# Optimization experiments

Measured on AMD Instinct MI355X. Metric: run time of the kernel, lower is better.

The kernel has to match this reference:

```python
import jax, jax.numpy as jnp
import numpy as np

B, T, D = 8, 2048, 1024
DK, DV = 1024, 1024


def setup_inputs() -> dict:
    key = jax.random.key(0)
    ks = jax.random.split(key, 7)
    s = 1.0 / np.sqrt(D)
    return {
        "X": jax.random.normal(ks[0], (B, T, D), dtype=jnp.float32),
        "Wq": jax.random.uniform(ks[1], (D, DK), jnp.float32, -s, s),
        "bq": jax.random.uniform(ks[2], (DK,), jnp.float32, -s, s),
        "Wk": jax.random.uniform(ks[3], (D, DK), jnp.float32, -s, s),
        "bk": jax.random.uniform(ks[4], (DK,), jnp.float32, -s, s),
        "Wv": jax.random.uniform(ks[5], (D, DV), jnp.float32, -s, s),
        "bv": jax.random.uniform(ks[6], (DV,), jnp.float32, -s, s),
    }


def reference(X, Wq, bq, Wk, bk, Wv, bv):
    # relu-activated projections (note: original applies relu to Q, K, V; no 1/sqrt(d) scaling)
    Q = jax.nn.relu(jnp.einsum("btd,dk->btk", X, Wq) + bq)  # [B,T,DK]
    K = jax.nn.relu(jnp.einsum("btd,dk->btk", X, Wk) + bk)  # [B,T,DK]
    V = jax.nn.relu(jnp.einsum("btd,dv->btv", X, Wv) + bv)  # [B,T,DV]
    scores = jnp.einsum("btk,bsk->bts", Q, K)               # [B,T,S] query t attends over keys s
    attn = jax.nn.softmax(scores, axis=-1)
    return jnp.einsum("bts,bsv->btv", attn, V)              # [B,T,DV]
```

## Files before the change

kernel.cpp:

```cpp
#include <hip/hip_runtime.h>

typedef __bf16 bf16x8 __attribute__((ext_vector_type(8)));
typedef _Float16 f16x8 __attribute__((ext_vector_type(8)));
typedef float floatx4 __attribute__((ext_vector_type(4)));

__device__ __forceinline__ unsigned short f2bf(float f) {
  unsigned int u = __float_as_uint(f);
  u += 0x7FFFu + ((u >> 16) & 1u);
  return (unsigned short)(u >> 16);
}
__device__ __forceinline__ unsigned short f2h(float f) {
  _Float16 h = (_Float16)f;
  return __builtin_bit_cast(unsigned short, h);
}
template <bool F16>
__device__ __forceinline__ unsigned short f2x(float f) {
  return F16 ? f2h(f) : f2bf(f);
}

__device__ __forceinline__ void g2l16(const void* g, void* l) {
  __builtin_amdgcn_global_load_lds(
      (const __attribute__((address_space(1))) void*)g,
      (__attribute__((address_space(3))) void*)l, 16, 0, 0);
}

template <int MODE, bool AF32, bool INF16, bool OUTF16>
__global__ __launch_bounds__(256) void gemm_bt(
    const void* __restrict__ Av, int lda, long sA,
    const unsigned short* __restrict__ B, int ldb, long sB,
    void* __restrict__ Cv, int ldc, long sC,
    int K, const float* __restrict__ bias, float* __restrict__ lrow) {
  __shared__ unsigned short As[2][128 * 64];
  __shared__ unsigned short Bs[2][128 * 64];
  const int tid = threadIdx.x;
  const int wave = tid >> 6, lane = tid & 63;
  const int z = blockIdx.z;
  const unsigned short* A16 = (const unsigned short*)Av + (size_t)z * sA;
  const float* A32 = (const float*)Av + (size_t)z * sA;
  B += (size_t)z * sB;

  int bx = blockIdx.x, by = blockIdx.y;
  {
    const int nwg = gridDim.x * gridDim.y;
    if ((nwg & 7) == 0) {
      int flat = by * gridDim.x + bx;
      flat = (flat & 7) * (nwg >> 3) + (flat >> 3);
      bx = flat % gridDim.x;
      by = flat / gridDim.x;
    }
  }
  const int m0 = by * 128, n0 = bx * 128;
  const int wr = (wave >> 1) * 64;
  const int wc = (wave & 1) * 64;
  const int qr = lane >> 4, lr = lane & 15;
  floatx4 acc[4][4] = {};

  auto stageAB = [&](int t, int buf) {
    const int k0 = t << 6;
#pragma unroll
    for (int it = 0; it < 4; ++it) {
      const int base = it * 256 + wave * 64;
      const int idx = base + lane;
      const int row = idx >> 3;
      const int gs = (idx & 7) ^ (row & 7);
      g2l16(A16 + (size_t)(m0 + row) * lda + k0 + gs * 8, &As[buf][base * 8]);
    }
#pragma unroll
    for (int it = 0; it < 4; ++it) {
      const int base = it * 256 + wave * 64;
      const int idx = base + lane;
      const int row = idx >> 3;
      const int gs = (idx & 7) ^ (row & 7);
      g2l16(B + (size_t)(n0 + row) * ldb + k0 + gs * 8, &Bs[buf][base * 8]);
    }
  };

  auto computeT = [&](int buf) {
#pragma unroll
    for (int kk = 0; kk < 64; kk += 32) {
      const int slot = (kk >> 3) + qr;
      if (INF16) {
        f16x8 af[4], bf[4];
#pragma unroll
        for (int i = 0; i < 4; ++i) {
          const int ra = wr + i * 16 + lr;
          af[i] = *(const f16x8*)&As[buf][ra * 64 + ((slot ^ (ra & 7)) * 8)];
        }
#pragma unroll
        for (int j = 0; j < 4; ++j) {
          const int rb = wc + j * 16 + lr;
          bf[j] = *(const f16x8*)&Bs[buf][rb * 64 + ((slot ^ (rb & 7)) * 8)];
        }
#pragma unroll
        for (int i = 0; i < 4; ++i)
#pragma unroll
          for (int j = 0; j < 4; ++j)
            acc[i][j] = __builtin_amdgcn_mfma_f32_16x16x32_f16(
                bf[j], af[i], acc[i][j], 0, 0, 0);
      } else {
        bf16x8 af[4], bf[4];
#pragma unroll
        for (int i = 0; i < 4; ++i) {
          const int ra = wr + i * 16 + lr;
          af[i] = *(const bf16x8*)&As[buf][ra * 64 + ((slot ^ (ra & 7)) * 8)];
        }
#pragma unroll
        for (int j = 0; j < 4; ++j) {
          const int rb = wc + j * 16 + lr;
          bf[j] = *(const bf16x8*)&Bs[buf][rb * 64 + ((slot ^ (rb & 7)) * 8)];
        }
#pragma unroll
        for (int i = 0; i < 4; ++i)
#pragma unroll
          for (int j = 0; j < 4; ++j)
            acc[i][j] = __builtin_amdgcn_mfma_f32_16x16x32_bf16(
                bf[j], af[i], acc[i][j], 0, 0, 0);
      }
    }
  };

  if (!AF32) {
    const int nk = K >> 6;
    stageAB(0, 0);
    for (int t = 0; t < nk; ++t) {
      const int cur = t & 1;
      if (t + 1 < nk) {
        stageAB(t + 1, cur ^ 1);
        asm volatile("s_waitcnt vmcnt(8)" ::: "memory");
      } else {
        asm volatile("s_waitcnt vmcnt(0)" ::: "memory");
      }
      __builtin_amdgcn_sched_barrier(0);
      __builtin_amdgcn_s_barrier();
      __builtin_amdgcn_sched_barrier(0);
      computeT(cur);
      __builtin_amdgcn_sched_barrier(0);
      __builtin_amdgcn_s_barrier();
      __builtin_amdgcn_sched_barrier(0);
    }
  } else {
    for (int k0 = 0; k0 < K; k0 += 64) {
      __syncthreads();
#pragma unroll
      for (int it = 0; it < 8; ++it) {
        const int idx = it * 256 + tid;
        const int row = idx >> 4, c4 = idx & 15;
        float4 v =
            *(const float4*)(A32 + (size_t)(m0 + row) * lda + k0 + c4 * 4);
        const int soff = (((c4 >> 1) ^ (row & 7)) * 2 + (c4 & 1)) * 4;
        *(ushort4*)&As[0][row * 64 + soff] =
            make_ushort4(f2x<INF16>(v.x), f2x<INF16>(v.y), f2x<INF16>(v.z),
                         f2x<INF16>(v.w));
      }
#pragma unroll
      for (int it = 0; it < 4; ++it) {
        const int base = it * 256 + wave * 64;
        const int idx = base + lane;
        const int row = idx >> 3;
        const int gs = (idx & 7) ^ (row & 7);
        g2l16(B + (size_t)(n0 + row) * ldb + k0 + gs * 8, &Bs[0][base * 8]);
      }
      __syncthreads();
      computeT(0);
    }
  }

  float* Cf = (float*)Cv + (size_t)z * sC;
  unsigned short* Cb = (unsigned short*)Cv + (size_t)z * sC;
#pragma unroll
  for (int i = 0; i < 4; ++i) {
    const int row = m0 + wr + i * 16 + lr;
    float rowsum = 0.0f;
    float invl = 1.0f;
    if (MODE == 2) invl = 1.0f / lrow[(size_t)z * 2048 + row];
#pragma unroll
    for (int j = 0; j < 4; ++j) {
      const int col0 = n0 + wc + j * 16 + qr * 4;
      if (MODE == 0) {
        float4 bj = *(const float4*)(bias + col0);
        float v0 = fmaxf(acc[i][j][0] + bj.x, 0.0f);
        float v1 = fmaxf(acc[i][j][1] + bj.y, 0.0f);
        float v2 = fmaxf(acc[i][j][2] + bj.z, 0.0f);
        float v3 = fmaxf(acc[i][j][3] + bj.w, 0.0f);
        *(ushort4*)&Cb[(size_t)row * ldc + col0] =
            make_ushort4(f2x<OUTF16>(v0), f2x<OUTF16>(v1), f2x<OUTF16>(v2),
                         f2x<OUTF16>(v3));
      } else if (MODE == 1) {
        float e0 = __expf(acc[i][j][0] - 60.0f);
        float e1 = __expf(acc[i][j][1] - 60.0f);
        float e2 = __expf(acc[i][j][2] - 60.0f);
        float e3 = __expf(acc[i][j][3] - 60.0f);
        *(ushort4*)&Cb[(size_t)row * ldc + col0] =
            make_ushort4(f2bf(e0), f2bf(e1), f2bf(e2), f2bf(e3));
        rowsum += (e0 + e1) + (e2 + e3);
      } else {
        *(float4*)&Cf[(size_t)row * ldc + col0] =
            make_float4(acc[i][j][0] * invl, acc[i][j][1] * invl,
                        acc[i][j][2] * invl, acc[i][j][3] * invl);
      }
    }
    if (MODE == 1) {
      rowsum += __shfl_xor(rowsum, 16);
      rowsum += __shfl_xor(rowsum, 32);
      if (lane < 16)
        atomicAdd(&lrow[(size_t)z * 2048 + row], rowsum);
    }
  }
}

template <bool F16>
__global__ __launch_bounds__(256) void cvt16(const float* __restrict__ in,
                                             unsigned short* __restrict__ out,
                                             int n) {
  const int i = (blockIdx.x * 256 + threadIdx.x) * 8;
  if (i >= n) return;
  float4 a = *(const float4*)(in + i);
  float4 b = *(const float4*)(in + i + 4);
  *(ushort4*)(out + i) =
      make_ushort4(f2x<F16>(a.x), f2x<F16>(a.y), f2x<F16>(a.z), f2x<F16>(a.w));
  *(ushort4*)(out + i + 4) =
      make_ushort4(f2x<F16>(b.x), f2x<F16>(b.y), f2x<F16>(b.z), f2x<F16>(b.w));
}

template <bool F16>
__global__ __launch_bounds__(256) void wtrans(const float* __restrict__ W,
                                              unsigned short* __restrict__ Wt) {
  __shared__ unsigned short t[64][68];
  const int tid = threadIdx.x;
  const int n0 = blockIdx.x * 64, k0 = blockIdx.y * 64;
#pragma unroll
  for (int it = 0; it < 4; ++it) {
    const int idx = it * 256 + tid;
    const int kr = idx >> 4, nq = idx & 15;
    float4 v = *(const float4*)&W[(size_t)(k0 + kr) * 1024 + n0 + nq * 4];
    t[kr][nq * 4 + 0] = f2x<F16>(v.x);
    t[kr][nq * 4 + 1] = f2x<F16>(v.y);
    t[kr][nq * 4 + 2] = f2x<F16>(v.z);
    t[kr][nq * 4 + 3] = f2x<F16>(v.w);
  }
  __syncthreads();
#pragma unroll
  for (int it = 0; it < 4; ++it) {
    const int idx = it * 256 + tid;
    const int nr = idx >> 4, kq = idx & 15;
    *(ushort4*)&Wt[(size_t)(n0 + nr) * 1024 + k0 + kq * 4] =
        make_ushort4(t[kq * 4 + 0][nr], t[kq * 4 + 1][nr],
                     t[kq * 4 + 2][nr], t[kq * 4 + 3][nr]);
  }
}

__global__ __launch_bounds__(256) void vtrans(const unsigned short* __restrict__ V,
                                              unsigned short* __restrict__ Vt) {
  __shared__ unsigned short t[64][68];
  const int tid = threadIdx.x;
  const int v0 = blockIdx.x * 64, t0 = blockIdx.y * 64;
  const int b = blockIdx.z;
  const unsigned short* Vb = V + (size_t)b * 2048 * 1024;
  unsigned short* Vtb = Vt + (size_t)b * 1024 * 2048;
#pragma unroll
  for (int it = 0; it < 4; ++it) {
    const int idx = it * 256 + tid;
    const int tr = idx >> 4, vq = idx & 15;
    ushort4 u = *(const ushort4*)&Vb[(size_t)(t0 + tr) * 1024 + v0 + vq * 4];
    t[tr][vq * 4 + 0] = u.x;
    t[tr][vq * 4 + 1] = u.y;
    t[tr][vq * 4 + 2] = u.z;
    t[tr][vq * 4 + 3] = u.w;
  }
  __syncthreads();
#pragma unroll
  for (int it = 0; it < 4; ++it) {
    const int idx = it * 256 + tid;
    const int vr = idx >> 4, tq = idx & 15;
    *(ushort4*)&Vtb[(size_t)(v0 + vr) * 2048 + t0 + tq * 4] =
        make_ushort4(t[tq * 4 + 0][vr], t[tq * 4 + 1][vr],
                     t[tq * 4 + 2][vr], t[tq * 4 + 3][vr]);
  }
}

__global__ void zero_f32(float* __restrict__ p, int n) {
  const int i = blockIdx.x * 256 + threadIdx.x;
  if (i < n) p[i] = 0.0f;
}

__global__ __launch_bounds__(256) void copy_half(const float* __restrict__ T,
                                                 float* __restrict__ out,
                                                 int roff) {
  const size_t i = ((size_t)blockIdx.x * 256 + threadIdx.x) * 4;
  const size_t b = i >> 20;
  const size_t rem = i & 1048575;
  float4 v = *(const float4*)(T + i);
  *(float4*)(out + b * 2097152 + (size_t)roff * 1024 + rem) = v;
}

__global__ void diag_ws(float* __restrict__ out, float mb) { out[0] = mb; }

extern "C" void kernel_launch(void* const* d_in, const int* in_sizes, int n_in,
                              void* d_out, int out_size, void* d_ws, size_t ws_size,
                              hipStream_t stream) {
  const float* X = (const float*)d_in[0];
  const float* Wq = (const float*)d_in[1];
  const float* bq = (const float*)d_in[2];
  const float* Wk = (const float*)d_in[3];
  const float* bk = (const float*)d_in[4];
  const float* Wv = (const float*)d_in[5];
  const float* bv = (const float*)d_in[6];
  float* out = (float*)d_out;
  char* ws = (char*)d_ws;
  const size_t MiB = 1ull << 20;

  const size_t B_WQT = 0, B_WKT = 2 * MiB, B_WVT = 4 * MiB;
  const size_t B_Q = 6 * MiB;
  const size_t B_K = 38 * MiB;
  const size_t B_E = 70 * MiB;
  const size_t B_L = 134 * MiB;
  const size_t NEEDED_BIG = B_L + 65536;

  const size_t S_WQT = 0, S_WKT = 2 * MiB, S_WVT = 4 * MiB;
  const size_t S_Q = 6 * MiB, S_K = 38 * MiB, S_L = 70 * MiB;
  const size_t NEEDED_SMALL = S_L + 65536;

  if (ws_size >= NEEDED_BIG) {
    unsigned short* Wqt = (unsigned short*)(ws + B_WQT);
    unsigned short* Wkt = (unsigned short*)(ws + B_WKT);
    unsigned short* Wvt = (unsigned short*)(ws + B_WVT);
    unsigned short* Q   = (unsigned short*)(ws + B_Q);
    unsigned short* Kb  = (unsigned short*)(ws + B_K);
    unsigned short* E   = (unsigned short*)(ws + B_E);
    float* l            = (float*)(ws + B_L);
    unsigned short* Xh = (unsigned short*)d_out;
    unsigned short* V  = (unsigned short*)d_out + 16384ull * 1024;

    cvt16<true><<<8192, 256, 0, stream>>>(X, Xh, 16384 * 1024);
    wtrans<true><<<dim3(16, 16), 256, 0, stream>>>(Wq, Wqt);
    wtrans<true><<<dim3(16, 16), 256, 0, stream>>>(Wk, Wkt);
    wtrans<true><<<dim3(16, 16), 256, 0, stream>>>(Wv, Wvt);
    zero_f32<<<64, 256, 0, stream>>>(l, 16384);

    gemm_bt<0, false, true, true><<<dim3(8, 128, 1), 256, 0, stream>>>(
        Xh, 1024, 0, Wqt, 1024, 0, Q, 1024, 0, 1024, bq, nullptr);
    gemm_bt<0, false, true, true><<<dim3(8, 128, 1), 256, 0, stream>>>(
        Xh, 1024, 0, Wkt, 1024, 0, Kb, 1024, 0, 1024, bk, nullptr);
    gemm_bt<0, false, true, false><<<dim3(8, 128, 1), 256, 0, stream>>>(
        Xh, 1024, 0, Wvt, 1024, 0, V, 1024, 0, 1024, bv, nullptr);

    gemm_bt<1, false, true, false><<<dim3(16, 16, 8), 256, 0, stream>>>(
        Q, 1024, 2048L * 1024, Kb, 1024, 2048L * 1024,
        E, 2048, 2048L * 2048, 1024, nullptr, l);

    vtrans<<<dim3(16, 32, 8), 256, 0, stream>>>(V, Q);

    gemm_bt<2, false, false, false><<<dim3(8, 16, 8), 256, 0, stream>>>(
        E, 2048, 2048L * 2048, Q, 2048, 1024L * 2048,
        out, 1024, 2048L * 1024, 2048, nullptr, l);
    return;
  }

  if (ws_size < NEEDED_SMALL) {
    diag_ws<<<1, 1, 0, stream>>>(out, (float)(ws_size >> 20));
    return;
  }

  unsigned short* Wqt = (unsigned short*)(ws + S_WQT);
  unsigned short* Wkt = (unsigned short*)(ws + S_WKT);
  unsigned short* Wvt = (unsigned short*)(ws + S_WVT);
  unsigned short* Q   = (unsigned short*)(ws + S_Q);
  unsigned short* Kb  = (unsigned short*)(ws + S_K);
  float* l            = (float*)(ws + S_L);
  unsigned short* Xh = (unsigned short*)d_out;
  unsigned short* E  = (unsigned short*)d_out;

  cvt16<true><<<8192, 256, 0, stream>>>(X, Xh, 16384 * 1024);
  wtrans<true><<<dim3(16, 16), 256, 0, stream>>>(Wq, Wqt);
  wtrans<true><<<dim3(16, 16), 256, 0, stream>>>(Wk, Wkt);
  wtrans<true><<<dim3(16, 16), 256, 0, stream>>>(Wv, Wvt);
  zero_f32<<<64, 256, 0, stream>>>(l, 16384);

  gemm_bt<0, false, true, true><<<dim3(8, 128, 1), 256, 0, stream>>>(
      Xh, 1024, 0, Wqt, 1024, 0, Q, 1024, 0, 1024, bq, nullptr);
  gemm_bt<0, false, true, true><<<dim3(8, 128, 1), 256, 0, stream>>>(
      Xh, 1024, 0, Wkt, 1024, 0, Kb, 1024, 0, 1024, bk, nullptr);

  gemm_bt<1, false, true, false><<<dim3(16, 16, 8), 256, 0, stream>>>(
      Q, 1024, 2048L * 1024, Kb, 1024, 2048L * 1024,
      E, 2048, 2048L * 2048, 1024, nullptr, l);

  gemm_bt<0, true, true, false><<<dim3(8, 128, 1), 256, 0, stream>>>(
      X, 1024, 0, Wvt, 1024, 0, Kb, 1024, 0, 1024, bv, nullptr);

  vtrans<<<dim3(16, 32, 8), 256, 0, stream>>>(Kb, Q);

  float* T = (float*)Kb;
  gemm_bt<2, false, false, false><<<dim3(8, 8, 8), 256, 0, stream>>>(
      E, 2048, 2048L * 2048, Q, 2048, 1024L * 2048,
      T, 1024, 1024L * 1024, 2048, nullptr, l);
  copy_half<<<8192, 256, 0, stream>>>(T, out, 0);
  gemm_bt<2, false, false, false><<<dim3(8, 8, 8), 256, 0, stream>>>(
      E + 1024L * 2048, 2048, 2048L * 2048, Q, 2048, 1024L * 2048,
      T, 1024, 1024L * 1024, 2048, nullptr, l + 1024);
  copy_half<<<8192, 256, 0, stream>>>(T, out, 1024);
}
```

Baseline: 443.4 us.

## Replace 128x128 GEMM with 256x256 tile, 8-wave kernel with phased pipelining

Adds a new gemm256 kernel that uses 256x256 output tiles, 512 threads, and a double-buffered LDS. Each K-tile is split into four quadrant phases that interleave staging of the next tile with MFMA work, and MFMA sections are wrapped in s_setprio. All non-fp32 GEMMs in both workspace paths now use this kernel. The goal is higher arithmetic intensity per LDS and global byte and better overlap of loads with compute. The trade-offs are 128KB of LDS per block, a large accumulator register footprint, and fewer blocks per grid, which could hurt occupancy or tail balance.

```diff
diff --git a/kernel.cpp b/kernel.cpp
--- a/kernel.cpp
+++ b/kernel.cpp
@@ -24,19 +24,89 @@
       (__attribute__((address_space(3))) void*)l, 16, 0, 0);
 }
 
-template <int MODE, bool AF32, bool INF16, bool OUTF16>
-__global__ __launch_bounds__(256) void gemm_bt(
-    const void* __restrict__ Av, int lda, long sA,
+template <bool F16> struct ABsel { using t = bf16x8; };
+template <> struct ABsel<true> { using t = f16x8; };
+__device__ __forceinline__ floatx4 mfma_ab(f16x8 b, f16x8 a, floatx4 c) {
+  return __builtin_amdgcn_mfma_f32_16x16x32_f16(b, a, c, 0, 0, 0);
+}
+__device__ __forceinline__ floatx4 mfma_ab(bf16x8 b, bf16x8 a, floatx4 c) {
+  return __builtin_amdgcn_mfma_f32_16x16x32_bf16(b, a, c, 0, 0, 0);
+}
+
+
+#define STAGE(C, TT, BD)                                                       \
+  {                                                                            \
+    const int k0s = (TT) << 6;                                                 \
+    _Pragma("unroll") for (int it = 0; it < 2; ++it) {                         \
+      const int cr0 = it * 64 + wave * 8;     \
+      int rb;                                                                  \
+      if ((C) == 0)                                                            \
+        rb = (cr0 < 64) ? cr0 : cr0 + 64;                                      \
+      else if ((C) == 3)                                                       \
+        rb = ((cr0 < 64) ? cr0 : cr0 + 64) + 64;                               \
+      else if ((C) == 1)                                                       \
+        rb = (cr0 & 31) + (cr0 >> 5) * 64;                                     \
+      else                                                                     \
+        rb = (cr0 & 31) + (cr0 >> 5) * 64 + 32;                                \
+      const int rl = rb + (lane >> 3);             \
+      const int gs = (lane & 7) ^ (lane >> 3);      \
+      if ((C) == 0 || (C) == 3)                                                \
+        g2l16(A + (size_t)(m0 + rl) * lda + k0s + gs * 8, &As[BD][rb * 64]);   \
+      else                                                                     \
+        g2l16(B + (size_t)(n0 + rl) * ldb + k0s + gs * 8, &Bs[BD][rb * 64]);   \
+    }                                                                          \
+  }
+
+#define LOADA(MH, BD)                                                          \
+  _Pragma("unroll") for (int i = 0; i < 4; ++i) {                              \
+    const int ra = wr + (MH) * 64 + i * 16 + lr;                               \
+    _Pragma("unroll") for (int ks = 0; ks < 2; ++ks) {                         \
+      const int sl = ks * 4 + qr;                                              \
+      af[i][ks] = *(const AB8*)&As[BD][ra * 64 + ((sl ^ (ra & 7)) * 8)];       \
+    }                                                                          \
+  }
+
+#define LOADB(DST, NH, BD)                                                     \
+  _Pragma("unroll") for (int j = 0; j < 2; ++j) {                              \
+    const int rq = wc + (NH) * 32 + j * 16 + lr;                               \
+    _Pragma("unroll") for (int ks = 0; ks < 2; ++ks) {                         \
+      const int sl = ks * 4 + qr;                                              \
+      DST[j][ks] = *(const AB8*)&Bs[BD][rq * 64 + ((sl ^ (rq & 7)) * 8)];      \
+    }                                                                          \
+  }
+
+#define MMAQ(MH, NH, BF)                                                       \
+  __builtin_amdgcn_s_setprio(1);                                               \
+  _Pragma("unroll") for (int ks = 0; ks < 2; ++ks)                             \
+      _Pragma("unroll") for (int i = 0; i < 4; ++i)                            \
+          _Pragma("unroll") for (int j = 0; j < 2; ++j)                        \
+              acc[(MH) * 4 + i][(NH) * 2 + j] = mfma_ab(                       \
+                  BF[j][ks], af[i][ks], acc[(MH) * 4 + i][(NH) * 2 + j]);      \
+  __builtin_amdgcn_s_setprio(0);
+
+#define GATE(N)                                                                \
+  __builtin_amdgcn_sched_barrier(0);                                           \
+  asm volatile("s_waitcnt vmcnt(" #N ")" ::: "memory");                        \
+  __builtin_amdgcn_s_barrier();                                                \
+  __builtin_amdgcn_sched_barrier(0);
+
+#define PHEND                                                                  \
+  __builtin_amdgcn_sched_barrier(0);                                           \
+  __builtin_amdgcn_s_barrier();                                                \
+  __builtin_amdgcn_sched_barrier(0);
+
+template <int MODE, bool INF16, bool OUTF16>
+__global__ __launch_bounds__(512, 2) void gemm256(
+    const unsigned short* __restrict__ A, int lda, long sA,
     const unsigned short* __restrict__ B, int ldb, long sB,
     void* __restrict__ Cv, int ldc, long sC,
     int K, const float* __restrict__ bias, float* __restrict__ lrow) {
-  __shared__ unsigned short As[2][128 * 64];
-  __shared__ unsigned short Bs[2][128 * 64];
+  __shared__ unsigned short As[2][256 * 64];
+  __shared__ unsigned short Bs[2][256 * 64];
   const int tid = threadIdx.x;
   const int wave = tid >> 6, lane = tid & 63;
   const int z = blockIdx.z;
-  const unsigned short* A16 = (const unsigned short*)Av + (size_t)z * sA;
-  const float* A32 = (const float*)Av + (size_t)z * sA;
+  A += (size_t)z * sA;
   B += (size_t)z * sB;
 
   int bx = blockIdx.x, by = blockIdx.y;
@@ -49,119 +119,168 @@
       by = flat / gridDim.x;
     }
   }
+  const int m0 = by * 256, n0 = bx * 256;
+  const int wr = (wave >> 2) * 128;
+  const int wc = (wave & 3) * 64;
+  const int qr = lane >> 4, lr = lane & 15;
+  using AB8 = typename ABsel<INF16>::t;
+  floatx4 acc[8][4] = {};
+  AB8 af[4][2], b0[2][2], b1[2][2];
+
+  const int nt = K >> 6;
+  STAGE(0, 0, 0) STAGE(1, 0, 0) STAGE(2, 0, 0) STAGE(3, 0, 0)
+
+  for (int t = 0; t < nt - 1; ++t) {
+    const int d = t & 1, e = d ^ 1;
+    STAGE(0, t + 1, e)
+    GATE(6)
+    LOADA(0, d) LOADB(b0, 0, d)
+    MMAQ(0, 0, b0)
+    PHEND
+    STAGE(1, t + 1, e)
+    GATE(6)
+    LOADB(b1, 1, d)
+    MMAQ(0, 1, b1)
+    PHEND
+    STAGE(2, t + 1, e)
+    GATE(6)
+    LOADA(1, d)
+    MMAQ(1, 1, b1)
+    PHEND
+    STAGE(3, t + 1, e)
+    __builtin_amdgcn_sched_barrier(0);
+    MMAQ(1, 0, b0)
+    PHEND
+  }
+  {
+    const int t = nt - 1, d = t & 1;
+    GATE(4)
+    LOADA(0, d) LOADB(b0, 0, d)
+    MMAQ(0, 0, b0)
+    PHEND
+    GATE(2)
+    LOADB(b1, 1, d)
+    MMAQ(0, 1, b1)
+    PHEND
+    GATE(0)
+    LOADA(1, d)
+    MMAQ(1, 1, b1)
+    PHEND
+    MMAQ(1, 0, b0)
+  }
+
+  float* Cf = (float*)Cv + (size_t)z * sC;
+  unsigned short* Cb = (unsigned short*)Cv + (size_t)z * sC;
+#pragma unroll
+  for (int mi = 0; mi < 8; ++mi) {
+    const int row = m0 + wr + mi * 16 + lr;
+    float rowsum = 0.0f;
+    float invl = 1.0f;
+    if (MODE == 2) invl = 1.0f / lrow[(size_t)z * 2048 + row];
+#pragma unroll
+    for (int nj = 0; nj < 4; ++nj) {
+      const int col0 = n0 + wc + nj * 16 + qr * 4;
+      if (MODE == 0) {
+        float4 bj = *(const float4*)(bias + col0);
+        float v0 = fmaxf(acc[mi][nj][0] + bj.x, 0.0f);
+        float v1 = fmaxf(acc[mi][nj][1] + bj.y, 0.0f);
+        float v2 = fmaxf(acc[mi][nj][2] + bj.z, 0.0f);
+        float v3 = fmaxf(acc[mi][nj][3] + bj.w, 0.0f);
+        *(ushort4*)&Cb[(size_t)row * ldc + col0] =
+            make_ushort4(f2x<OUTF16>(v0), f2x<OUTF16>(v1), f2x<OUTF16>(v2),
+                         f2x<OUTF16>(v3));
+      } else if (MODE == 1) {
+        float e0 = __expf(acc[mi][nj][0] - 60.0f);
+        float e1 = __expf(acc[mi][nj][1] - 60.0f);
+        float e2 = __expf(acc[mi][nj][2] - 60.0f);
+        float e3 = __expf(acc[mi][nj][3] - 60.0f);
+        *(ushort4*)&Cb[(size_t)row * ldc + col0] =
+            make_ushort4(f2bf(e0), f2bf(e1), f2bf(e2), f2bf(e3));
+        rowsum += (e0 + e1) + (e2 + e3);
+      } else {
+        *(float4*)&Cf[(size_t)row * ldc + col0] =
+            make_float4(acc[mi][nj][0] * invl, acc[mi][nj][1] * invl,
+                        acc[mi][nj][2] * invl, acc[mi][nj][3] * invl);
+      }
+    }
+    if (MODE == 1) {
+      rowsum += __shfl_xor(rowsum, 16);
+      rowsum += __shfl_xor(rowsum, 32);
+      if (lane < 16) atomicAdd(&lrow[(size_t)z * 2048 + row], rowsum);
+    }
+  }
+}
+
+template <int MODE, bool AF32, bool INF16, bool OUTF16>
+__global__ __launch_bounds__(256) void gemm_bt(
+    const void* __restrict__ Av, int lda, long sA,
+    const unsigned short* __restrict__ B, int ldb, long sB,
+    void* __restrict__ Cv, int ldc, long sC,
+    int K, const float* __restrict__ bias, float* __restrict__ lrow) {
+  __shared__ unsigned short Asl[128 * 64];
+  __shared__ unsigned short Bsl[128 * 64];
+  const int tid = threadIdx.x;
+  const int wave = tid >> 6, lane = tid & 63;
+  const int z = blockIdx.z;
+  const float* A32 = (const float*)Av + (size_t)z * sA;
+  B += (size_t)z * sB;
+  int bx = blockIdx.x, by = blockIdx.y;
+  {
+    const int nwg = gridDim.x * gridDim.y;
+    if ((nwg & 7) == 0) {
+      int flat = by * gridDim.x + bx;
+      flat = (flat & 7) * (nwg >> 3) + (flat >> 3);
+      bx = flat % gridDim.x;
+      by = flat / gridDim.x;
+    }
+  }
   const int m0 = by * 128, n0 = bx * 128;
   const int wr = (wave >> 1) * 64;
   const int wc = (wave & 1) * 64;
   const int qr = lane >> 4, lr = lane & 15;
   floatx4 acc[4][4] = {};
 
-  auto stageAB = [&](int t, int buf) {
-    const int k0 = t << 6;
+  for (int k0 = 0; k0 < K; k0 += 64) {
+    __syncthreads();
+#pragma unroll
+    for (int it = 0; it < 8; ++it) {
+      const int idx = it * 256 + tid;
+      const int row = idx >> 4, c4 = idx & 15;
+      float4 v = *(const float4*)(A32 + (size_t)(m0 + row) * lda + k0 + c4 * 4);
+      const int soff = (((c4 >> 1) ^ (row & 7)) * 2 + (c4 & 1)) * 4;
+      *(ushort4*)&Asl[row * 64 + soff] =
+          make_ushort4(f2x<INF16>(v.x), f2x<INF16>(v.y), f2x<INF16>(v.z),
+                       f2x<INF16>(v.w));
+    }
 #pragma unroll
     for (int it = 0; it < 4; ++it) {
       const int base = it * 256 + wave * 64;
       const int idx = base + lane;
       const int row = idx >> 3;
       const int gs = (idx & 7) ^ (row & 7);
-      g2l16(A16 + (size_t)(m0 + row) * lda + k0 + gs * 8, &As[buf][base * 8]);
-    }
-#pragma unroll
-    for (int it = 0; it < 4; ++it) {
-      const int base = it * 256 + wave * 64;
-      const int idx = base + lane;
-      const int row = idx >> 3;
-      const int gs = (idx & 7) ^ (row & 7);
-      g2l16(B + (size_t)(n0 + row) * ldb + k0 + gs * 8, &Bs[buf][base * 8]);
-    }
-  };
-
-  auto computeT = [&](int buf) {
+      g2l16(B + (size_t)(n0 + row) * ldb + k0 + gs * 8, &Bsl[base * 8]);
+    }
+    __syncthreads();
 #pragma unroll
     for (int kk = 0; kk < 64; kk += 32) {
       const int slot = (kk >> 3) + qr;
-      if (INF16) {
-        f16x8 af[4], bf[4];
-#pragma unroll
-        for (int i = 0; i < 4; ++i) {
-          const int ra = wr + i * 16 + lr;
-          af[i] = *(const f16x8*)&As[buf][ra * 64 + ((slot ^ (ra & 7)) * 8)];
-        }
-#pragma unroll
-        for (int j = 0; j < 4; ++j) {
-          const int rb = wc + j * 16 + lr;
-          bf[j] = *(const f16x8*)&Bs[buf][rb * 64 + ((slot ^ (rb & 7)) * 8)];
-        }
-#pragma unroll
-        for (int i = 0; i < 4; ++i)
-#pragma unroll
-          for (int j = 0; j < 4; ++j)
-            acc[i][j] = __builtin_amdgcn_mfma_f32_16x16x32_f16(
-                bf[j], af[i], acc[i][j], 0, 0, 0);
-      } else {
-        bf16x8 af[4], bf[4];
-#pragma unroll
-        for (int i = 0; i < 4; ++i) {
-          const int ra = wr + i * 16 + lr;
-          af[i] = *(const bf16x8*)&As[buf][ra * 64 + ((slot ^ (ra & 7)) * 8)];
-        }
-#pragma unroll
-        for (int j = 0; j < 4; ++j) {
-          const int rb = wc + j * 16 + lr;
-          bf[j] = *(const bf16x8*)&Bs[buf][rb * 64 + ((slot ^ (rb & 7)) * 8)];
-        }
-#pragma unroll
-        for (int i = 0; i < 4; ++i)
-#pragma unroll
-          for (int j = 0; j < 4; ++j)
-            acc[i][j] = __builtin_amdgcn_mfma_f32_16x16x32_bf16(
-                bf[j], af[i], acc[i][j], 0, 0, 0);
+      bf16x8 af[4], bf[4];
+#pragma unroll
+      for (int i = 0; i < 4; ++i) {
+        const int ra = wr + i * 16 + lr;
+        af[i] = *(const bf16x8*)&Asl[ra * 64 + ((slot ^ (ra & 7)) * 8)];
       }
-    }
-  };
-
-  if (!AF32) {
-    const int nk = K >> 6;
-    stageAB(0, 0);
-    for (int t = 0; t < nk; ++t) {
-      const int cur = t & 1;
-      if (t + 1 < nk) {
-        stageAB(t + 1, cur ^ 1);
-        asm volatile("s_waitcnt vmcnt(8)" ::: "memory");
-      } else {
-        asm volatile("s_waitcnt vmcnt(0)" ::: "memory");
+#pragma unroll
+      for (int j = 0; j < 4; ++j) {
+        const int rb = wc + j * 16 + lr;
+        bf[j] = *(const bf16x8*)&Bsl[rb * 64 + ((slot ^ (rb & 7)) * 8)];
       }
-      __builtin_amdgcn_sched_barrier(0);
-      __builtin_amdgcn_s_barrier();
-      __builtin_amdgcn_sched_barrier(0);
-      computeT(cur);
-      __builtin_amdgcn_sched_barrier(0);
-      __builtin_amdgcn_s_barrier();
-      __builtin_amdgcn_sched_barrier(0);
-    }
-  } else {
-    for (int k0 = 0; k0 < K; k0 += 64) {
-      __syncthreads();
-#pragma unroll
-      for (int it = 0; it < 8; ++it) {
-        const int idx = it * 256 + tid;
-        const int row = idx >> 4, c4 = idx & 15;
-        float4 v =
-            *(const float4*)(A32 + (size_t)(m0 + row) * lda + k0 + c4 * 4);
-        const int soff = (((c4 >> 1) ^ (row & 7)) * 2 + (c4 & 1)) * 4;
-        *(ushort4*)&As[0][row * 64 + soff] =
-            make_ushort4(f2x<INF16>(v.x), f2x<INF16>(v.y), f2x<INF16>(v.z),
-                         f2x<INF16>(v.w));
-      }
-#pragma unroll
-      for (int it = 0; it < 4; ++it) {
-        const int base = it * 256 + wave * 64;
-        const int idx = base + lane;
-        const int row = idx >> 3;
-        const int gs = (idx & 7) ^ (row & 7);
-        g2l16(B + (size_t)(n0 + row) * ldb + k0 + gs * 8, &Bs[0][base * 8]);
-      }
-      __syncthreads();
-      computeT(0);
+#pragma unroll
+      for (int i = 0; i < 4; ++i)
+#pragma unroll
+        for (int j = 0; j < 4; ++j)
+          acc[i][j] = __builtin_amdgcn_mfma_f32_16x16x32_bf16(bf[j], af[i],
+                                                              acc[i][j], 0, 0, 0);
     }
   }
 
@@ -202,8 +321,7 @@
     if (MODE == 1) {
       rowsum += __shfl_xor(rowsum, 16);
       rowsum += __shfl_xor(rowsum, 32);
-      if (lane < 16)
-        atomicAdd(&lrow[(size_t)z * 2048 + row], rowsum);
+      if (lane < 16) atomicAdd(&lrow[(size_t)z * 2048 + row], rowsum);
     }
   }
 }
@@ -337,20 +455,20 @@
     wtrans<true><<<dim3(16, 16), 256, 0, stream>>>(Wv, Wvt);
     zero_f32<<<64, 256, 0, stream>>>(l, 16384);
 
-    gemm_bt<0, false, true, true><<<dim3(8, 128, 1), 256, 0, stream>>>(
+    gemm256<0, true, true><<<dim3(4, 64, 1), 512, 0, stream>>>(
         Xh, 1024, 0, Wqt, 1024, 0, Q, 1024, 0, 1024, bq, nullptr);
-    gemm_bt<0, false, true, true><<<dim3(8, 128, 1), 256, 0, stream>>>(
+    gemm256<0, true, true><<<dim3(4, 64, 1), 512, 0, stream>>>(
         Xh, 1024, 0, Wkt, 1024, 0, Kb, 1024, 0, 1024, bk, nullptr);
-    gemm_bt<0, false, true, false><<<dim3(8, 128, 1), 256, 0, stream>>>(
+    gemm256<0, true, false><<<dim3(4, 64, 1), 512, 0, stream>>>(
         Xh, 1024, 0, Wvt, 1024, 0, V, 1024, 0, 1024, bv, nullptr);
 
-    gemm_bt<1, false, true, false><<<dim3(16, 16, 8), 256, 0, stream>>>(
+    gemm256<1, true, false><<<dim3(8, 8, 8), 512, 0, stream>>>(
         Q, 1024, 2048L * 1024, Kb, 1024, 2048L * 1024,
         E, 2048, 2048L * 2048, 1024, nullptr, l);
 
     vtrans<<<dim3(16, 32, 8), 256, 0, stream>>>(V, Q);
 
-    gemm_bt<2, false, false, false><<<dim3(8, 16, 8), 256, 0, stream>>>(
+    gemm256<2, false, false><<<dim3(4, 8, 8), 512, 0, stream>>>(
         E, 2048, 2048L * 2048, Q, 2048, 1024L * 2048,
         out, 1024, 2048L * 1024, 2048, nullptr, l);
     return;
@@ -376,12 +494,12 @@
   wtrans<true><<<dim3(16, 16), 256, 0, stream>>>(Wv, Wvt);
   zero_f32<<<64, 256, 0, stream>>>(l, 16384);
 
-  gemm_bt<0, false, true, true><<<dim3(8, 128, 1), 256, 0, stream>>>(
+  gemm256<0, true, true><<<dim3(4, 64, 1), 512, 0, stream>>>(
       Xh, 1024, 0, Wqt, 1024, 0, Q, 1024, 0, 1024, bq, nullptr);
-  gemm_bt<0, false, true, true><<<dim3(8, 128, 1), 256, 0, stream>>>(
+  gemm256<0, true, true><<<dim3(4, 64, 1), 512, 0, stream>>>(
       Xh, 1024, 0, Wkt, 1024, 0, Kb, 1024, 0, 1024, bk, nullptr);
 
-  gemm_bt<1, false, true, false><<<dim3(16, 16, 8), 256, 0, stream>>>(
+  gemm256<1, true, false><<<dim3(8, 8, 8), 512, 0, stream>>>(
       Q, 1024, 2048L * 1024, Kb, 1024, 2048L * 1024,
       E, 2048, 2048L * 2048, 1024, nullptr, l);
 
@@ -391,11 +509,11 @@
   vtrans<<<dim3(16, 32, 8), 256, 0, stream>>>(Kb, Q);
 
   float* T = (float*)Kb;
-  gemm_bt<2, false, false, false><<<dim3(8, 8, 8), 256, 0, stream>>>(
+  gemm256<2, false, false><<<dim3(4, 4, 8), 512, 0, stream>>>(
       E, 2048, 2048L * 2048, Q, 2048, 1024L * 2048,
       T, 1024, 1024L * 1024, 2048, nullptr, l);
   copy_half<<<8192, 256, 0, stream>>>(T, out, 0);
-  gemm_bt<2, false, false, false><<<dim3(8, 8, 8), 256, 0, stream>>>(
+  gemm256<2, false, false><<<dim3(4, 4, 8), 512, 0, stream>>>(
       E + 1024L * 2048, 2048, 2048L * 2048, Q, 2048, 1024L * 2048,
       T, 1024, 1024L * 1024, 2048, nullptr, l + 1024);
   copy_half<<<8192, 256, 0, stream>>>(T, out, 1024);
```

Measured after the change: 471.1 us. +6.3%, slower.
